# Performance work log

Hardware: AMD Instinct MI355X
Metric: run time of the kernel (lower is better)

## Reference

```python
import jax, jax.numpy as jnp
import numpy as np

# Mamba2 hyperparams (mamba_ssm defaults given __init__ args)
D_MODEL = 512
FF = 2048
D_STATE = 128
D_CONV = 4
EXPAND = 2
D_INNER = EXPAND * D_MODEL          # 1024
HEADDIM = 64
NHEADS = D_INNER // HEADDIM         # 16
NGROUPS = 1
CONV_DIM = D_INNER + 2 * NGROUPS * D_STATE       # 1280
D_IN_PROJ = 2 * D_INNER + 2 * NGROUPS * D_STATE + NHEADS  # 2320
CHUNK = 128
EPS = 1e-5


def setup_inputs() -> dict:
    key = jax.random.key(0)
    ks = jax.random.split(key, 16)
    B, S = 8, 2048
    s = 0.02
    dt_init = jax.random.uniform(ks[4], (NHEADS,), minval=0.001, maxval=0.1)
    return {
        # forward args (dropout treated as eval / identity)
        "tgt": jax.random.normal(ks[0], (B, S, D_MODEL), jnp.float32),
        "memory": jax.random.normal(ks[1], (B, 256, D_MODEL), jnp.float32),
        "spatial_shapes": jnp.array([[16, 16]], jnp.int32),
        "level_start_index": jnp.array([0], jnp.int32),
        "valid_ratios": jnp.ones((B, 1, 2), jnp.float32),
        # Mamba2 params
        "in_proj_w": jax.random.normal(ks[2], (D_IN_PROJ, D_MODEL), jnp.float32) * s,
        "conv_w": jax.random.normal(ks[3], (CONV_DIM, D_CONV), jnp.float32) * s,
        "conv_b": jnp.zeros((CONV_DIM,), jnp.float32),
        "dt_bias": jnp.log(jnp.expm1(dt_init)),  # inverse softplus of dt_init
        "A_log": jnp.log(jax.random.uniform(ks[5], (NHEADS,), minval=1.0, maxval=16.0)),
        "D_head": jnp.ones((NHEADS,), jnp.float32),
        "norm_w": jnp.ones((D_INNER,), jnp.float32),
        "out_proj_w": jax.random.normal(ks[6], (D_MODEL, D_INNER), jnp.float32) * s,
        # LayerNorms + FFN
        "norm1_w": jnp.ones((D_MODEL,)), "norm1_b": jnp.zeros((D_MODEL,)),
        "w1": jax.random.normal(ks[7], (FF, D_MODEL), jnp.float32) * s,
        "b1": jnp.zeros((FF,)),
        "w2": jax.random.normal(ks[8], (D_MODEL, FF), jnp.float32) * s,
        "b2": jnp.zeros((D_MODEL,)),
        "norm3_w": jnp.ones((D_MODEL,)), "norm3_b": jnp.zeros((D_MODEL,)),
    }


def _layer_norm(x, w, b):
    m = jnp.mean(x, -1, keepdims=True)
    v = jnp.mean((x - m) ** 2, -1, keepdims=True)
    return (x - m) * jax.lax.rsqrt(v + EPS) * w + b


def _ssd(x, dt, A, Bm, Cm):
    # chunked selective-scan (SSD). x:(b,s,h,p) dt:(b,s,h) A:(h,) Bm,Cm:(b,s,n)
    b, s, h, p = x.shape
    n = Bm.shape[-1]
    c, l = s // CHUNK, CHUNK
    x = x.reshape(b, c, l, h, p)
    dt = dt.reshape(b, c, l, h)
    Bm = Bm.reshape(b, c, l, n)
    Cm = Cm.reshape(b, c, l, n)
    a_cs = jnp.cumsum(dt * A, axis=2)                 # (b,c,l,h) cumulative log-decay
    ac = a_cs.transpose(0, 1, 3, 2)                   # (b,c,h,l)
    mask = jnp.tril(jnp.ones((l, l), bool))
    Lmat = jnp.exp(jnp.where(mask, ac[..., :, None] - ac[..., None, :], -jnp.inf))
    # intra-chunk (causal) contribution
    Y_diag = jnp.einsum('bcin,bcjn,bchij,bcjh,bcjhp->bcihp', Cm, Bm, Lmat, dt, x)
    # per-chunk final states
    decay_end = jnp.exp(a_cs[:, :, -1:, :] - a_cs)    # (b,c,l,h)
    states = jnp.einsum('bcln,bclh,bclh,bclhp->bchpn', Bm, decay_end, dt, x)
    chunk_decay = jnp.exp(a_cs[:, :, -1, :])          # (b,c,h)
    def step(h0, inp):
        cd, st = inp
        return cd[:, :, None, None] * h0 + st, h0
    h_init = jnp.zeros((b, h, p, n), x.dtype)
    _, prev = jax.lax.scan(step, h_init,
                           (chunk_decay.transpose(1, 0, 2),
                            states.transpose(1, 0, 2, 3, 4)))
    prev = prev.transpose(1, 0, 2, 3, 4)              # (b,c,h,p,n) state at chunk start
    Y_off = jnp.einsum('bcln,bchpn,bclh->bclhp', Cm, prev, jnp.exp(a_cs))
    return (Y_diag + Y_off).reshape(b, s, h, p)


def _mamba2(u, in_proj_w, conv_w, conv_b, dt_bias, A_log, D_head, norm_w, out_proj_w):
    Bb, S, _ = u.shape
    zxbcdt = u @ in_proj_w.T                          # (b,s,2320)
    z, xBC, dt = jnp.split(zxbcdt, [D_INNER, D_INNER + CONV_DIM], axis=-1)
    # causal depthwise conv1d + silu
    xp = jnp.pad(xBC, ((0, 0), (D_CONV - 1, 0), (0, 0)))
    conv = sum(xp[:, k:k + S, :] * conv_w[:, k] for k in range(D_CONV)) + conv_b
    xBC = jax.nn.silu(conv)
    x, Bm, Cm = jnp.split(xBC, [D_INNER, D_INNER + NGROUPS * D_STATE], axis=-1)
    dt = jax.nn.softplus(dt + dt_bias)                # (b,s,h)
    A = -jnp.exp(A_log)                               # (h,)
    x = x.reshape(Bb, S, NHEADS, HEADDIM)
    y = _ssd(x, dt, A, Bm, Cm) + D_head[None, None, :, None] * x
    y = y.reshape(Bb, S, D_INNER)
    # gated RMSNorm: rmsnorm(y * silu(z)) * w
    y = y * jax.nn.silu(z)
    y = y * jax.lax.rsqrt(jnp.mean(y * y, -1, keepdims=True) + EPS) * norm_w
    return y @ out_proj_w.T


def reference(tgt, memory, spatial_shapes, level_start_index, valid_ratios,
              in_proj_w, conv_w, conv_b, dt_bias, A_log, D_head, norm_w, out_proj_w,
              norm1_w, norm1_b, w1, b1, w2, b2, norm3_w, norm3_b):
    t2 = _mamba2(tgt, in_proj_w, conv_w, conv_b, dt_bias, A_log, D_head, norm_w, out_proj_w)
    t = _layer_norm(tgt + t2, norm1_w, norm1_b)
    ff = jax.nn.gelu(t @ w1.T + b1, approximate=False) @ w2.T + b2
    return _layer_norm(t + ff, norm3_w, norm3_b)
```

## Files before the change

### kernel.cpp

```cpp
#include <hip/hip_runtime.h>
#include <hip/hip_bf16.h>
#include <math.h>


namespace {
constexpr int BB = 8;
constexpr int S = 2048;
constexpr int DM = 512;
constexpr int DIP = 2320;
constexpr int DIPP = 2432;
constexpr int DI = 1024;
constexpr int CDIM = 1280;
constexpr int NH = 16;
constexpr int HD = 64;
constexpr int DSTATE = 128;
constexpr int CH = 128;
constexpr int NC = S / CH;
constexpr int FF = 2048;
constexpr float EPS = 1e-5f;
constexpr int LP = 132;
}

using bf16_t = __hip_bfloat16;
typedef __attribute__((ext_vector_type(8))) short short8;
typedef __attribute__((ext_vector_type(4))) float f32x4;

__device__ __forceinline__ float gelu_exact(float x) {
    return 0.5f * x * (1.0f + erff(x * 0.7071067811865476f));
}
__device__ __forceinline__ unsigned short f2bfu(float f) {
    bf16_t b = __float2bfloat16(f);
    return *(unsigned short*)&b;
}
__device__ __forceinline__ float bfu2f(unsigned short u) {
    union { unsigned int i; float f; } v; v.i = (unsigned)u << 16; return v.f;
}

__device__ __forceinline__ void block_sum2(float& a, float& b) {
    #pragma unroll
    for (int o = 32; o > 0; o >>= 1) {
        a += __shfl_down(a, o, 64);
        b += __shfl_down(b, o, 64);
    }
    __shared__ float sa[4], sb[4];
    int w = threadIdx.x >> 6;
    if ((threadIdx.x & 63) == 0) { sa[w] = a; sb[w] = b; }
    __syncthreads();
    a = sa[0] + sa[1] + sa[2] + sa[3];
    b = sb[0] + sb[1] + sb[2] + sb[3];
}

template <int BM, int BK, int ACT, bool HASBIAS, bool OUTBF>
__global__ __launch_bounds__(256)
void mfma_gemm(const bf16_t* __restrict__ A, const bf16_t* __restrict__ W,
               const float* __restrict__ bias, void* __restrict__ Cout,
               int N, int K, int lda, int ldw, int ldc,
               long batchA, long batchW, long batchC)
{
    A += (long)blockIdx.z * batchA;
    W += (long)blockIdx.z * batchW;
    constexpr int NJ = (BM == 128) ? 4 : 2;
    constexpr int KO = BK / 32;
    constexpr int QA = 256 / BM;
    constexpr int TA = (BM * BK) / 2048;
    constexpr int TW = (128 * BK) / 2048;
    __shared__ bf16_t As[2][BM * BK];
    __shared__ bf16_t Ws[2][128 * BK];
    const int tid = threadIdx.x;
    const int lane = tid & 63;
    const int wave = tid >> 6;

    const int nwg = gridDim.x * gridDim.y;
    int wgid = blockIdx.y * gridDim.x + blockIdx.x;
    if ((nwg & 7) == 0) {
        const int q = nwg >> 3;
        wgid = (wgid & 7) * q + (wgid >> 3);
    }
    const int bxi = wgid % gridDim.x;
    const int byi = wgid / gridDim.x;
    const long bm = (long)byi * BM;
    const int bn = bxi * 128;

    const int rA = tid & (BM - 1);
    const int qA = tid / BM;
    const int rW = tid & 127;
    const int qW = tid >> 7;
    const bf16_t* Ag = A + (bm + rA) * (long)lda + qA * 8;
    const bf16_t* Wg = W + ((long)bn + rW) * (long)ldw + qW * 8;
    const int laoff = (qA * BM + rA) * 8;
    const int lwoff = (qW * 128 + rW) * 8;

    const int kq = lane >> 4;
    const int lr = lane & 15;
    const int wm = (BM == 128) ? (wave & 1) * 64 : 0;
    const int wn = (BM == 128) ? (wave >> 1) * 64 : wave * 32;

    f32x4 acc[4][NJ];
    #pragma unroll
    for (int i = 0; i < 4; i++)
        #pragma unroll
        for (int j = 0; j < NJ; j++) acc[i][j] = (f32x4){0.f, 0.f, 0.f, 0.f};

    short8 raA[TA], rwA[TW];
    short8 raB[TA], rwB[TW];
    const int nt = K / BK;

    #pragma unroll
    for (int u = 0; u < TA; u++) raA[u] = *(const short8*)(Ag + u * (QA * 8));
    #pragma unroll
    for (int u = 0; u < TW; u++) rwA[u] = *(const short8*)(Wg + u * 16);
    #pragma unroll
    for (int u = 0; u < TA; u++) *(short8*)&As[0][laoff + u * (QA * BM * 8)] = raA[u];
    #pragma unroll
    for (int u = 0; u < TW; u++) *(short8*)&Ws[0][lwoff + u * 2048] = rwA[u];
    if (nt > 1) {
        #pragma unroll
        for (int u = 0; u < TA; u++) raB[u] = *(const short8*)(Ag + BK + u * (QA * 8));
        #pragma unroll
        for (int u = 0; u < TW; u++) rwB[u] = *(const short8*)(Wg + BK + u * 16);
    }

    for (int t = 0; t < nt; t += 2) {
        if (t + 2 < nt) {
            const long ko = (long)(t + 2) * BK;
            #pragma unroll
            for (int u = 0; u < TA; u++) raA[u] = *(const short8*)(Ag + ko + u * (QA * 8));
            #pragma unroll
            for (int u = 0; u < TW; u++) rwA[u] = *(const short8*)(Wg + ko + u * 16);
        }
        __syncthreads();
        #pragma unroll
        for (int hk = 0; hk < KO; hk++) {
            short8 af[4], bfr[NJ];
            #pragma unroll
            for (int i = 0; i < 4; i++)
                af[i] = *(const short8*)&As[0][((hk * 4 + kq) * BM + wm + i * 16 + lr) * 8];
            #pragma unroll
            for (int j = 0; j < NJ; j++)
                bfr[j] = *(const short8*)&Ws[0][((hk * 4 + kq) * 128 + wn + j * 16 + lr) * 8];
            #pragma unroll
            for (int i = 0; i < 4; i++)
                #pragma unroll
                for (int j = 0; j < NJ; j++)
                    acc[i][j] = __builtin_amdgcn_mfma_f32_16x16x32_bf16(af[i], bfr[j], acc[i][j], 0, 0, 0);
        }
        #pragma unroll
        for (int u = 0; u < TA; u++) *(short8*)&As[1][laoff + u * (QA * BM * 8)] = raB[u];
        #pragma unroll
        for (int u = 0; u < TW; u++) *(short8*)&Ws[1][lwoff + u * 2048] = rwB[u];

        if (t + 3 < nt) {
            const long ko = (long)(t + 3) * BK;
            #pragma unroll
            for (int u = 0; u < TA; u++) raB[u] = *(const short8*)(Ag + ko + u * (QA * 8));
            #pragma unroll
            for (int u = 0; u < TW; u++) rwB[u] = *(const short8*)(Wg + ko + u * 16);
        }
        __syncthreads();
        #pragma unroll
        for (int hk = 0; hk < KO; hk++) {
            short8 af[4], bfr[NJ];
            #pragma unroll
            for (int i = 0; i < 4; i++)
                af[i] = *(const short8*)&As[1][((hk * 4 + kq) * BM + wm + i * 16 + lr) * 8];
            #pragma unroll
            for (int j = 0; j < NJ; j++)
                bfr[j] = *(const short8*)&Ws[1][((hk * 4 + kq) * 128 + wn + j * 16 + lr) * 8];
            #pragma unroll
            for (int i = 0; i < 4; i++)
                #pragma unroll
                for (int j = 0; j < NJ; j++)
                    acc[i][j] = __builtin_amdgcn_mfma_f32_16x16x32_bf16(af[i], bfr[j], acc[i][j], 0, 0, 0);
        }
        if (t + 2 < nt) {
            #pragma unroll
            for (int u = 0; u < TA; u++) *(short8*)&As[0][laoff + u * (QA * BM * 8)] = raA[u];
            #pragma unroll
            for (int u = 0; u < TW; u++) *(short8*)&Ws[0][lwoff + u * 2048] = rwA[u];
        }
    }

    const bool addb = HASBIAS && (blockIdx.z == 0);
    #pragma unroll
    for (int i = 0; i < 4; i++) {
        #pragma unroll
        for (int j = 0; j < NJ; j++) {
            int col = bn + wn + j * 16 + lr;
            if (col < N) {
                float bv = addb ? bias[col] : 0.f;
                #pragma unroll
                for (int r = 0; r < 4; r++) {
                    long row = bm + wm + i * 16 + kq * 4 + r;
                    float v = acc[i][j][r] + bv;
                    if (ACT == 1) v = gelu_exact(v);
                    if (OUTBF) ((bf16_t*)Cout)[row * (long)ldc + col + blockIdx.z * batchC] = __float2bfloat16(v);
                    else       ((float*)Cout)[row * (long)ldc + col + blockIdx.z * batchC] = v;
                }
            }
        }
    }
}

__global__ __launch_bounds__(256)
void dt_cvt(const float* __restrict__ tgt, const float* __restrict__ Wdt,
            const float* __restrict__ dt_bias, bf16_t* __restrict__ tgt_bf,
            float* __restrict__ dts)
{
    const int lane = threadIdx.x & 63;
    const int wave = threadIdx.x >> 6;
    float Wl[16][8];
    #pragma unroll
    for (int h = 0; h < 16; h++) {
        float4 a = *(const float4*)&Wdt[h * 512 + lane * 8];
        float4 b = *(const float4*)&Wdt[h * 512 + lane * 8 + 4];
        Wl[h][0] = a.x; Wl[h][1] = a.y; Wl[h][2] = a.z; Wl[h][3] = a.w;
        Wl[h][4] = b.x; Wl[h][5] = b.y; Wl[h][6] = b.z; Wl[h][7] = b.w;
    }
    float bs[16];
    #pragma unroll
    for (int h = 0; h < 16; h++) bs[h] = dt_bias[h];

    const long row0 = ((long)blockIdx.x * 4 + wave) * 4;
    #pragma unroll
    for (int rr = 0; rr < 4; rr++) {
        const long t = row0 + rr;
        float4 xa = *(const float4*)&tgt[t * 512 + lane * 8];
        float4 xb = *(const float4*)&tgt[t * 512 + lane * 8 + 4];
        float x[8] = {xa.x, xa.y, xa.z, xa.w, xb.x, xb.y, xb.z, xb.w};
        short8 ob;
        #pragma unroll
        for (int q = 0; q < 8; q++) ob[q] = (short)f2bfu(x[q]);
        *(short8*)&tgt_bf[t * 512 + lane * 8] = ob;

        float acc[16];
        #pragma unroll
        for (int h = 0; h < 16; h++) {
            float s = 0.f;
            #pragma unroll
            for (int q = 0; q < 8; q++) s += x[q] * Wl[h][q];
            acc[h] = s;
        }
        #pragma unroll
        for (int off = 32; off > 0; off >>= 1)
            #pragma unroll
            for (int h = 0; h < 16; h++)
                acc[h] += __shfl_xor(acc[h], off, 64);
        if (lane == 0) {
            #pragma unroll
            for (int h = 0; h < 16; h++) {
                float v = acc[h] + bs[h];
                dts[t * NH + h] = (v > 20.f) ? v : log1pf(__expf(v));
            }
        }
    }
}

__global__ __launch_bounds__(256)
void cvt_bf16(const float* __restrict__ s, bf16_t* __restrict__ d, long n)
{
    long i = ((long)blockIdx.x * 256 + threadIdx.x) * 4;
    if (i >= n) return;
    float4 v = *(const float4*)(s + i);
    d[i + 0] = __float2bfloat16(v.x);
    d[i + 1] = __float2bfloat16(v.y);
    d[i + 2] = __float2bfloat16(v.z);
    d[i + 3] = __float2bfloat16(v.w);
}

__global__ __launch_bounds__(256)
void cvt_bf16_pad(const float* __restrict__ s, bf16_t* __restrict__ d,
                  int rows_src, long total, int cols)
{
    long i = (long)blockIdx.x * 256 + threadIdx.x;
    if (i >= total) return;
    long r = i / cols;
    d[i] = __float2bfloat16(r < rows_src ? s[i] : 0.f);
}

__global__ __launch_bounds__(256)
void conv_silu_t16(const bf16_t* __restrict__ zx, const float* __restrict__ cw,
                   const float* __restrict__ cb, bf16_t* __restrict__ xBC)
{
    const int quad = blockIdx.x * 64 + (threadIdx.x & 63);
    const int wv = threadIdx.x >> 6;
    const int c = quad * 4;
    const int s0 = blockIdx.y * 64 + wv * 16;
    const long t0 = (long)blockIdx.z * S + s0;

    float wgt[4][4];
    #pragma unroll
    for (int cc = 0; cc < 4; cc++)
        #pragma unroll
        for (int k = 0; k < 4; k++) wgt[cc][k] = cw[(c + cc) * 4 + k];
    float bias[4];
    #pragma unroll
    for (int cc = 0; cc < 4; cc++) bias[cc] = cb[c + cc];

    unsigned long long rows[19];
    #pragma unroll
    for (int i = 0; i < 19; i++) {
        int s = s0 + i - 3;
        rows[i] = (s >= 0) ? *(const unsigned long long*)&zx[(t0 + i - 3) * DIP + DI + c] : 0ULL;
    }
    #pragma unroll
    for (int i = 0; i < 16; i++) {
        float v[4];
        #pragma unroll
        for (int cc = 0; cc < 4; cc++) v[cc] = bias[cc];
        #pragma unroll
        for (int k = 0; k < 4; k++) {
            unsigned long long u = rows[i + k];
            v[0] += bfu2f((unsigned short)(u      )) * wgt[0][k];
            v[1] += bfu2f((unsigned short)(u >> 16)) * wgt[1][k];
            v[2] += bfu2f((unsigned short)(u >> 32)) * wgt[2][k];
            v[3] += bfu2f((unsigned short)(u >> 48)) * wgt[3][k];
        }
        unsigned long long o = 0;
        #pragma unroll
        for (int cc = 0; cc < 4; cc++) {
            float sv = v[cc] / (1.f + __expf(-v[cc]));
            o |= (unsigned long long)f2bfu(sv) << (16 * cc);
        }
        *(unsigned long long*)&xBC[(t0 + i) * (long)CDIM + c] = o;
    }
}

__global__ __launch_bounds__(256)
void ssd_states(const bf16_t* __restrict__ xBC, const float* __restrict__ dts,
                const float* __restrict__ A_log,
                float* __restrict__ st, float* __restrict__ acs_all,
                float* __restrict__ cdlog)
{
    const int bid = blockIdx.x;
    const int nh = bid & 1;
    const int h = (bid >> 1) & 15;
    const int c = (bid >> 5) & 15;
    const int b = bid >> 9;
    const int sbid = (b * NC + c) * NH + h;
    const int tid = threadIdx.x;
    const int lane = tid & 63;
    const int wave = tid >> 6;
    __shared__ float dtv[128];
    __shared__ float acs[128];
    __shared__ float wj[128];
    __shared__ bf16_t XT[64 * LP];
    __shared__ bf16_t BwT[64 * LP];
    const long t0 = (long)b * S + (long)c * CH;
    const float Ah = -__expf(A_log[h]);

    if (tid < 128) {
        float d = dts[(t0 + tid) * NH + h];
        dtv[tid] = d;
        acs[tid] = d * Ah;
    }
    __syncthreads();
    for (int off = 1; off < 128; off <<= 1) {
        float add = 0.f;
        if (tid < 128 && tid >= off) add = acs[tid - off];
        __syncthreads();
        if (tid < 128 && tid >= off) acs[tid] += add;
        __syncthreads();
    }
    const float el = acs[127];
    if (tid < 128) wj[tid] = __expf(el - acs[tid]) * dtv[tid];
    if (nh == 0) {
        if (tid < 128) acs_all[(long)sbid * 128 + tid] = acs[tid];
        if (tid == 0) cdlog[sbid] = el;
    }
    __syncthreads();

    const int n0b = nh * 64;
    for (int i = tid; i < 4096; i += 256) {
        int p = i & 63, jp = (i >> 6) << 1;
        unsigned short a = *(const unsigned short*)&xBC[(t0 + jp) * CDIM + h * HD + p];
        unsigned short bb = *(const unsigned short*)&xBC[(t0 + jp + 1) * CDIM + h * HD + p];
        *(unsigned int*)&XT[p * LP + jp] = (unsigned)a | ((unsigned)bb << 16);
    }
    for (int i = tid; i < 4096; i += 256) {
        int n = i & 63, jp = (i >> 6) << 1;
        float v0 = __bfloat162float(xBC[(t0 + jp) * CDIM + DI + n0b + n]) * wj[jp];
        float v1 = __bfloat162float(xBC[(t0 + jp + 1) * CDIM + DI + n0b + n]) * wj[jp + 1];
        *(unsigned int*)&BwT[n * LP + jp] = (unsigned)f2bfu(v0) | ((unsigned)f2bfu(v1) << 16);
    }
    __syncthreads();

    const int kq = lane >> 4;
    const int lr = lane & 15;
    const int p0w = (wave & 1) * 32;
    const int n0w = (wave >> 1) * 32;
    f32x4 acc[2][2];
    #pragma unroll
    for (int i = 0; i < 2; i++)
        #pragma unroll
        for (int j = 0; j < 2; j++) acc[i][j] = (f32x4){0.f, 0.f, 0.f, 0.f};
    #pragma unroll
    for (int t = 0; t < 4; t++) {
        short8 af[2], bfr[2];
        #pragma unroll
        for (int i = 0; i < 2; i++)
            af[i] = *(const short8*)&XT[(p0w + i * 16 + lr) * LP + t * 32 + kq * 8];
        #pragma unroll
        for (int j = 0; j < 2; j++)
            bfr[j] = *(const short8*)&BwT[(n0w + j * 16 + lr) * LP + t * 32 + kq * 8];
        #pragma unroll
        for (int i = 0; i < 2; i++)
            #pragma unroll
            for (int j = 0; j < 2; j++)
                acc[i][j] = __builtin_amdgcn_mfma_f32_16x16x32_bf16(af[i], bfr[j], acc[i][j], 0, 0, 0);
    }
    long base = (long)sbid * 8192;
    #pragma unroll
    for (int i = 0; i < 2; i++)
        #pragma unroll
        for (int j = 0; j < 2; j++) {
            int col = n0b + n0w + j * 16 + lr;
            #pragma unroll
            for (int r = 0; r < 4; r++) {
                int p = p0w + i * 16 + kq * 4 + r;
                st[base + p * 128 + col] = acc[i][j][r];
            }
        }
}

__global__ __launch_bounds__(256)
void ssd_scan(const float* __restrict__ st, const float* __restrict__ cdlog,
              bf16_t* __restrict__ prevb)
{
    const int h = blockIdx.x & 15;
    const int b = blockIdx.x >> 4;
    const int q0 = blockIdx.y * 8;
    const int tid = threadIdx.x;
    float prev[8];
    #pragma unroll
    for (int q = 0; q < 8; q++) prev[q] = 0.f;
    for (int c = 0; c < NC; c++) {
        int bc = (b * NC + c) * NH + h;
        float cd = __expf(cdlog[bc]);
        long base = (long)bc * 8192 + (long)q0 * 256;
        #pragma unroll
        for (int q = 0; q < 8; q++) {
            long idx = base + (long)q * 256 + tid;
            float v = st[idx];
            prevb[idx] = __float2bfloat16(prev[q]);
            prev[q] = cd * prev[q] + v;
        }
    }
}

__global__ __launch_bounds__(256)
void ssd_out(const bf16_t* __restrict__ xBC, const float* __restrict__ dts,
             const bf16_t* __restrict__ G, const bf16_t* __restrict__ prevb,
             const float* __restrict__ acs_all, const float* __restrict__ D_head,
             bf16_t* __restrict__ y)
{
    const int bid = blockIdx.x;
    const int ih = bid & 1;
    const int h = (bid >> 1) & 15;
    const int c = (bid >> 5) & 15;
    const int b = bid >> 9;
    const int sbid = (b * NC + c) * NH + h;
    const int tid = threadIdx.x;
    const int lane = tid & 63;
    const int wave = tid >> 6;
    __shared__ float dtv[128];
    __shared__ float acs[128];
    __shared__ float eacs[64];
    __shared__ bf16_t Abuf[64 * LP];
    __shared__ bf16_t Bbuf[64 * LP];
    const long t0 = (long)b * S + (long)c * CH;
    const int m0b = ih * 64;

    if (tid < 128) {
        dtv[tid] = dts[(t0 + tid) * NH + h];
        acs[tid] = acs_all[(long)sbid * 128 + tid];
    }
    __syncthreads();
    if (tid < 64) eacs[tid] = __expf(acs[m0b + tid]);

    const bf16_t* Gb = G + (long)(b * NC + c) * 128 * 128;
    for (int i = tid; i < 4096; i += 256) {
        int rl = i >> 6, kp = (i & 63) << 1;
        int grow = m0b + rl;
        unsigned int g2 = *(const unsigned int*)&Gb[grow * 128 + kp];
        float w0 = (kp     <= grow) ? bfu2f((unsigned short)(g2      )) * __expf(acs[grow] - acs[kp    ]) * dtv[kp    ] : 0.f;
        float w1 = (kp + 1 <= grow) ? bfu2f((unsigned short)(g2 >> 16)) * __expf(acs[grow] - acs[kp + 1]) * dtv[kp + 1] : 0.f;
        *(unsigned int*)&Abuf[rl * LP + kp] = (unsigned)f2bfu(w0) | ((unsigned)f2bfu(w1) << 16);
    }
    for (int i = tid; i < 4096; i += 256) {
        int p = i & 63, jp = (i >> 6) << 1;
        unsigned short a = *(const unsigned short*)&xBC[(t0 + jp) * CDIM + h * HD + p];
        unsigned short bb = *(const unsigned short*)&xBC[(t0 + jp + 1) * CDIM + h * HD + p];
        *(unsigned int*)&Bbuf[p * LP + jp] = (unsigned)a | ((unsigned)bb << 16);
    }
    __syncthreads();

    const int kq = lane >> 4;
    const int lr = lane & 15;
    const int m0w = (wave & 1) * 32;
    const int p0 = (wave >> 1) * 32;
    f32x4 acc[2][2];
    #pragma unroll
    for (int i = 0; i < 2; i++)
        #pragma unroll
        for (int j = 0; j < 2; j++) acc[i][j] = (f32x4){0.f, 0.f, 0.f, 0.f};

    #pragma unroll
    for (int t = 0; t < 4; t++) {
        short8 af[2], bfr[2];
        #pragma unroll
        for (int i = 0; i < 2; i++)
            af[i] = *(const short8*)&Abuf[(m0w + i * 16 + lr) * LP + t * 32 + kq * 8];
        #pragma unroll
        for (int j = 0; j < 2; j++)
            bfr[j] = *(const short8*)&Bbuf[(p0 + j * 16 + lr) * LP + t * 32 + kq * 8];
        #pragma unroll
        for (int i = 0; i < 2; i++)
            #pragma unroll
            for (int j = 0; j < 2; j++)
                acc[i][j] = __builtin_amdgcn_mfma_f32_16x16x32_bf16(af[i], bfr[j], acc[i][j], 0, 0, 0);
    }
    const float Dh = D_head[h];
    float dx[2][2][4];
    #pragma unroll
    for (int i = 0; i < 2; i++)
        #pragma unroll
        for (int j = 0; j < 2; j++) {
            int col = p0 + j * 16 + lr;
            #pragma unroll
            for (int r = 0; r < 4; r++) {
                int rl = m0w + i * 16 + kq * 4 + r;
                dx[i][j][r] = Dh * __bfloat162float(Bbuf[col * LP + m0b + rl]);
            }
        }
    __syncthreads();

    for (int i = tid; i < 4096; i += 256) {
        int rl = i >> 6, np = (i & 63) << 1;
        unsigned int c2 = *(const unsigned int*)&xBC[(t0 + m0b + rl) * CDIM + DI + DSTATE + np];
        float e = eacs[rl];
        float v0 = e * bfu2f((unsigned short)(c2      ));
        float v1 = e * bfu2f((unsigned short)(c2 >> 16));
        *(unsigned int*)&Abuf[rl * LP + np] = (unsigned)f2bfu(v0) | ((unsigned)f2bfu(v1) << 16);
    }
    for (int i = tid; i < 4096; i += 256) {
        int p = i >> 6, np = (i & 63) << 1;
        *(unsigned int*)&Bbuf[p * LP + np] =
            *(const unsigned int*)&prevb[(long)sbid * 8192 + p * 128 + np];
    }
    __syncthreads();

    #pragma unroll
    for (int t = 0; t < 4; t++) {
        short8 af[2], bfr[2];
        #pragma unroll
        for (int i = 0; i < 2; i++)
            af[i] = *(const short8*)&Abuf[(m0w + i * 16 + lr) * LP + t * 32 + kq * 8];
        #pragma unroll
        for (int j = 0; j < 2; j++)
            bfr[j] = *(const short8*)&Bbuf[(p0 + j * 16 + lr) * LP + t * 32 + kq * 8];
        #pragma unroll
        for (int i = 0; i < 2; i++)
            #pragma unroll
            for (int j = 0; j < 2; j++)
                acc[i][j] = __builtin_amdgcn_mfma_f32_16x16x32_bf16(af[i], bfr[j], acc[i][j], 0, 0, 0);
    }

    #pragma unroll
    for (int i = 0; i < 2; i++)
        #pragma unroll
        for (int j = 0; j < 2; j++) {
            int col = p0 + j * 16 + lr;
            #pragma unroll
            for (int r = 0; r < 4; r++) {
                int rl = m0w + i * 16 + kq * 4 + r;
                y[(t0 + m0b + rl) * DI + h * HD + col] = __float2bfloat16(acc[i][j][r] + dx[i][j][r]);
            }
        }
}

__global__ __launch_bounds__(256)
void gated_rms(const bf16_t* __restrict__ y, const bf16_t* __restrict__ zx,
               const float* __restrict__ norm_w, bf16_t* __restrict__ yn)
{
    const long t = blockIdx.x;
    const int d = threadIdx.x * 4;
    unsigned long long zu = *(const unsigned long long*)&zx[t * DIP + d];
    unsigned long long yu = *(const unsigned long long*)&y[t * DI + d];
    float g[4];
    float ss = 0.f, dummy = 0.f;
    #pragma unroll
    for (int q = 0; q < 4; q++) {
        float zv = bfu2f((unsigned short)(zu >> (16 * q)));
        float yv = bfu2f((unsigned short)(yu >> (16 * q)));
        float gv = yv * (zv / (1.f + __expf(-zv)));
        g[q] = gv;
        ss += gv * gv;
    }
    block_sum2(ss, dummy);
    float scale = rsqrtf(ss * (1.f / DI) + EPS);
    unsigned long long o = 0;
    #pragma unroll
    for (int q = 0; q < 4; q++)
        o |= (unsigned long long)f2bfu(g[q] * scale * norm_w[d + q]) << (16 * q);
    *(unsigned long long*)&yn[t * DI + d] = o;
}

template <bool W16>
__global__ __launch_bounds__(256)
void add_ln(const float* __restrict__ x, const float* __restrict__ r,
            const float* __restrict__ w, const float* __restrict__ bpar,
            float* __restrict__ o32, bf16_t* __restrict__ o16)
{
    const int tid = threadIdx.x;
    const long t = blockIdx.x * 2 + (tid >> 7);
    const int i = (tid & 127) * 4;
    float4 xv = *(const float4*)(x + t * DM + i);
    float4 rv = *(const float4*)(r + t * DM + i);
    float v[4] = {xv.x + rv.x, xv.y + rv.y, xv.z + rv.z, xv.w + rv.w};
    float s = v[0] + v[1] + v[2] + v[3];
    float s2 = v[0]*v[0] + v[1]*v[1] + v[2]*v[2] + v[3]*v[3];
    #pragma unroll
    for (int o = 32; o > 0; o >>= 1) {
        s += __shfl_down(s, o, 64);
        s2 += __shfl_down(s2, o, 64);
    }
    __shared__ float sa[4], sb[4];
    int wv = tid >> 6;
    if ((tid & 63) == 0) { sa[wv] = s; sb[wv] = s2; }
    __syncthreads();
    int base = (tid >> 7) * 2;
    s = sa[base] + sa[base + 1];
    s2 = sb[base] + sb[base + 1];
    float mean = s * (1.f / DM);
    float var = s2 * (1.f / DM) - mean * mean;
    float inv = rsqrtf(var + EPS);
    float4 ov;
    float* op = (float*)&ov;
    unsigned long long o16u = 0;
    #pragma unroll
    for (int q = 0; q < 4; q++) {
        float o = (v[q] - mean) * inv * w[i + q] + bpar[i + q];
        op[q] = o;
        if (W16) o16u |= (unsigned long long)f2bfu(o) << (16 * q);
    }
    *(float4*)(o32 + t * DM + i) = ov;
    if (W16) *(unsigned long long*)&o16[t * DM + i] = o16u;
}


extern "C" void kernel_launch(void* const* d_in, const int* in_sizes, int n_in,
                              void* d_out, int out_size, void* d_ws, size_t ws_size,
                              hipStream_t stream)
{
    const float* tgt       = (const float*)d_in[0];
    const float* in_proj_w = (const float*)d_in[5];
    const float* conv_w    = (const float*)d_in[6];
    const float* conv_b    = (const float*)d_in[7];
    const float* dt_bias   = (const float*)d_in[8];
    const float* A_log     = (const float*)d_in[9];
    const float* D_head    = (const float*)d_in[10];
    const float* norm_w    = (const float*)d_in[11];
    const float* out_proj_w= (const float*)d_in[12];
    const float* norm1_w   = (const float*)d_in[13];
    const float* norm1_b   = (const float*)d_in[14];
    const float* w1        = (const float*)d_in[15];
    const float* b1        = (const float*)d_in[16];
    const float* w2        = (const float*)d_in[17];
    const float* b2        = (const float*)d_in[18];
    const float* norm3_w   = (const float*)d_in[19];
    const float* norm3_b   = (const float*)d_in[20];
    float* out = (float*)d_out;

    float* ws = (float*)d_ws;

    const size_t SZ_INW  = (size_t)DIPP * DM / 2;
    const size_t SZ_OUTW = (size_t)DM * DI / 2;
    const size_t SZ_W1   = (size_t)FF * DM / 2;
    const size_t SZ_W2   = (size_t)DM * FF / 2;
    size_t wo = 0;
    bf16_t* inW  = (bf16_t*)(ws + wo); wo += SZ_INW;
    bf16_t* outW = (bf16_t*)(ws + wo); wo += SZ_OUTW;
    bf16_t* w1b  = (bf16_t*)(ws + wo); wo += SZ_W1;
    bf16_t* w2b  = (bf16_t*)(ws + wo); wo += SZ_W2;
    const size_t WB = wo;

    const size_t PB = (size_t)S * DM / 2
                    + (size_t)S * DIP / 2
                    + (size_t)S * NH
                    + (size_t)S * CDIM / 2
                    + (size_t)NC * 128 * 128 / 2
                    + (size_t)NC * NH * 128
                    + (size_t)NC * NH
                    + (size_t)S * DI
                    + (size_t)S * DI;
    int NB = 0;
    for (int nb = 8; nb >= 1; nb >>= 1) {
        if (ws_size >= (WB + (size_t)nb * PB) * sizeof(float)) { NB = nb; break; }
    }
    if (NB == 0) return;

    {
        long n = (long)DIPP * DM;
        cvt_bf16_pad<<<(n + 255) / 256, 256, 0, stream>>>(in_proj_w, inW, DIP, n, DM);
        n = (long)DM * DI;
        cvt_bf16<<<(n / 4 + 255) / 256, 256, 0, stream>>>(out_proj_w, outW, n);
        n = (long)FF * DM;
        cvt_bf16<<<(n / 4 + 255) / 256, 256, 0, stream>>>(w1, w1b, n);
        n = (long)DM * FF;
        cvt_bf16<<<(n / 4 + 255) / 256, 256, 0, stream>>>(w2, w2b, n);
    }

    for (int b0 = 0; b0 < BB; b0 += NB) {
        const long Tg = (long)NB * S;
        size_t o = WB;
        bf16_t* tgt_bf = (bf16_t*)(ws + o); o += (size_t)Tg * DM / 2;
        bf16_t* zx     = (bf16_t*)(ws + o); o += (size_t)Tg * DIP / 2;
        float*  dts    = ws + o;            o += (size_t)Tg * NH;
        bf16_t* xBC    = (bf16_t*)(ws + o); o += (size_t)Tg * CDIM / 2;
        bf16_t* Gbuf   = (bf16_t*)(ws + o); o += (size_t)NB * NC * 128 * 128 / 2;
        float*  acs    = ws + o;            o += (size_t)NB * NC * NH * 128;
        float*  cdl    = ws + o;            o += (size_t)NB * NC * NH;
        float*  ybuf   = ws + o;            o += (size_t)Tg * DI;
        float*  st     = ws + o;            o += (size_t)Tg * DI;

        bf16_t* ybf   = (bf16_t*)ybuf;
        bf16_t* prevb = (bf16_t*)(ybuf + (size_t)Tg * DI / 2);
        bf16_t* yn  = (bf16_t*)st;
        float*  t2  = ybuf;
        float*  tb  = (float*)zx;
        bf16_t* tbb = (bf16_t*)(((float*)zx) + Tg * DM);
        bf16_t* h1  = (bf16_t*)ybuf;
        float*  fb  = (float*)xBC;

        const float* tgt_g = tgt + (long)b0 * S * DM;
        float* out_g = out + (long)b0 * S * DM;

        dt_cvt<<<Tg / 16, 256, 0, stream>>>(
            tgt_g, in_proj_w + (long)(DI + CDIM) * DM, dt_bias, tgt_bf, dts);
        mfma_gemm<128, 32, 0, false, true><<<dim3(DIPP / 128, Tg / 128, 1), 256, 0, stream>>>(
            tgt_bf, inW, nullptr, zx, DIP, DM, DM, DM, DIP, 0, 0, 0);
        conv_silu_t16<<<dim3(CDIM / 256, S / 64, NB), 256, 0, stream>>>(zx, conv_w, conv_b, xBC);
        mfma_gemm<128, 32, 0, false, true><<<dim3(1, 1, NB * NC), 256, 0, stream>>>(
            xBC + DI + DSTATE, xBC + DI, nullptr, Gbuf,
            128, DSTATE, CDIM, CDIM, 128,
            (long)CH * CDIM, (long)CH * CDIM, (long)128 * 128);
        ssd_states<<<NB * NC * NH * 2, 256, 0, stream>>>(xBC, dts, A_log, st, acs, cdl);
        ssd_scan<<<dim3(NB * NH, 4), 256, 0, stream>>>(st, cdl, prevb);
        ssd_out<<<NB * NC * NH * 2, 256, 0, stream>>>(xBC, dts, Gbuf, prevb, acs, D_head, ybf);
        gated_rms<<<Tg, 256, 0, stream>>>(ybf, zx, norm_w, yn);
        mfma_gemm<128, 32, 0, false, false><<<dim3(DM / 128, Tg / 128, 1), 256, 0, stream>>>(
            yn, outW, nullptr, t2, DM, DI, DI, DI, DM, 0, 0, 0);
        add_ln<true><<<Tg / 2, 256, 0, stream>>>(tgt_g, t2, norm1_w, norm1_b, tb, tbb);
        mfma_gemm<128, 32, 1, true, true><<<dim3(FF / 128, Tg / 128, 1), 256, 0, stream>>>(
            tbb, w1b, b1, h1, FF, DM, DM, DM, FF, 0, 0, 0);
        mfma_gemm<128, 32, 0, true, false><<<dim3(DM / 128, Tg / 128, 1), 256, 0, stream>>>(
            h1, w2b, b2, fb, DM, FF, FF, FF, DM, 0, 0, 0);
        add_ln<false><<<Tg / 2, 256, 0, stream>>>(tb, fb, norm3_w, norm3_b, out_g, nullptr);
    }
}
```

Before: 824.4 us.

## Merge SSD state and output half-blocks into one block per chunk-head

The SSD state and output kernels previously split each (batch, chunk, head) across two blocks. Each of those blocks redid the cumsum, the X transpose, and the G-weighting and D-term work for its half. Now a single block covers the whole 128-wide tile, with each wave computing a 2x4 MFMA tile, so the shared loads and exp computations are done once. The cumsum also switches from a shared-memory Hillis-Steele loop with many barriers to wave shuffles plus one cross-wave fixup. In exchange the grid has half as many blocks and each block uses more LDS and registers, which can lower occupancy and latency hiding.

```diff
diff --git a/kernel.cpp b/kernel.cpp
--- a/kernel.cpp
+++ b/kernel.cpp
@@ -326,16 +326,15 @@
 }
 
 __global__ __launch_bounds__(256)
-void ssd_states(const bf16_t* __restrict__ xBC, const float* __restrict__ dts,
-                const float* __restrict__ A_log,
-                float* __restrict__ st, float* __restrict__ acs_all,
-                float* __restrict__ cdlog)
+void ssd_states2(const bf16_t* __restrict__ xBC, const float* __restrict__ dts,
+                 const float* __restrict__ A_log,
+                 float* __restrict__ st, float* __restrict__ acs_all,
+                 float* __restrict__ cdlog)
 {
     const int bid = blockIdx.x;
-    const int nh = bid & 1;
-    const int h = (bid >> 1) & 15;
-    const int c = (bid >> 5) & 15;
-    const int b = bid >> 9;
+    const int h = bid & 15;
+    const int c = (bid >> 4) & 15;
+    const int b = bid >> 8;
     const int sbid = (b * NC + c) * NH + h;
     const int tid = threadIdx.x;
     const int lane = tid & 63;
@@ -343,43 +342,45 @@
     __shared__ float dtv[128];
     __shared__ float acs[128];
     __shared__ float wj[128];
+    __shared__ float wsum[2];
     __shared__ bf16_t XT[64 * LP];
-    __shared__ bf16_t BwT[64 * LP];
+    __shared__ bf16_t BwT[128 * LP];
     const long t0 = (long)b * S + (long)c * CH;
     const float Ah = -__expf(A_log[h]);
 
+    float dv = 0.f, x = 0.f;
     if (tid < 128) {
-        float d = dts[(t0 + tid) * NH + h];
-        dtv[tid] = d;
-        acs[tid] = d * Ah;
-    }
-    __syncthreads();
-    for (int off = 1; off < 128; off <<= 1) {
-        float add = 0.f;
-        if (tid < 128 && tid >= off) add = acs[tid - off];
-        __syncthreads();
-        if (tid < 128 && tid >= off) acs[tid] += add;
-        __syncthreads();
-    }
+        dv = dts[(t0 + tid) * NH + h];
+        x = dv * Ah;
+    }
+    #pragma unroll
+    for (int off = 1; off < 64; off <<= 1) {
+        float n = __shfl_up(x, off, 64);
+        if (lane >= off) x += n;
+    }
+    if (tid < 128 && lane == 63) wsum[tid >> 6] = x;
+    __syncthreads();
+    if (tid >= 64 && tid < 128) x += wsum[0];
+    if (tid < 128) { dtv[tid] = dv; acs[tid] = x; }
+    __syncthreads();
     const float el = acs[127];
-    if (tid < 128) wj[tid] = __expf(el - acs[tid]) * dtv[tid];
-    if (nh == 0) {
-        if (tid < 128) acs_all[(long)sbid * 128 + tid] = acs[tid];
-        if (tid == 0) cdlog[sbid] = el;
-    }
-    __syncthreads();
-
-    const int n0b = nh * 64;
+    if (tid < 128) {
+        wj[tid] = __expf(el - acs[tid]) * dtv[tid];
+        acs_all[(long)sbid * 128 + tid] = acs[tid];
+    }
+    if (tid == 0) cdlog[sbid] = el;
+    __syncthreads();
+
     for (int i = tid; i < 4096; i += 256) {
         int p = i & 63, jp = (i >> 6) << 1;
         unsigned short a = *(const unsigned short*)&xBC[(t0 + jp) * CDIM + h * HD + p];
         unsigned short bb = *(const unsigned short*)&xBC[(t0 + jp + 1) * CDIM + h * HD + p];
         *(unsigned int*)&XT[p * LP + jp] = (unsigned)a | ((unsigned)bb << 16);
     }
-    for (int i = tid; i < 4096; i += 256) {
-        int n = i & 63, jp = (i >> 6) << 1;
-        float v0 = __bfloat162float(xBC[(t0 + jp) * CDIM + DI + n0b + n]) * wj[jp];
-        float v1 = __bfloat162float(xBC[(t0 + jp + 1) * CDIM + DI + n0b + n]) * wj[jp + 1];
+    for (int i = tid; i < 8192; i += 256) {
+        int n = i & 127, jp = (i >> 7) << 1;
+        float v0 = __bfloat162float(xBC[(t0 + jp) * CDIM + DI + n]) * wj[jp];
+        float v1 = __bfloat162float(xBC[(t0 + jp + 1) * CDIM + DI + n]) * wj[jp + 1];
         *(unsigned int*)&BwT[n * LP + jp] = (unsigned)f2bfu(v0) | ((unsigned)f2bfu(v1) << 16);
     }
     __syncthreads();
@@ -387,33 +388,33 @@
     const int kq = lane >> 4;
     const int lr = lane & 15;
     const int p0w = (wave & 1) * 32;
-    const int n0w = (wave >> 1) * 32;
-    f32x4 acc[2][2];
+    const int n0w = (wave >> 1) * 64;
+    f32x4 acc[2][4];
     #pragma unroll
     for (int i = 0; i < 2; i++)
         #pragma unroll
-        for (int j = 0; j < 2; j++) acc[i][j] = (f32x4){0.f, 0.f, 0.f, 0.f};
+        for (int j = 0; j < 4; j++) acc[i][j] = (f32x4){0.f, 0.f, 0.f, 0.f};
     #pragma unroll
     for (int t = 0; t < 4; t++) {
-        short8 af[2], bfr[2];
+        short8 af[2], bfr[4];
         #pragma unroll
         for (int i = 0; i < 2; i++)
             af[i] = *(const short8*)&XT[(p0w + i * 16 + lr) * LP + t * 32 + kq * 8];
         #pragma unroll
-        for (int j = 0; j < 2; j++)
+        for (int j = 0; j < 4; j++)
             bfr[j] = *(const short8*)&BwT[(n0w + j * 16 + lr) * LP + t * 32 + kq * 8];
         #pragma unroll
         for (int i = 0; i < 2; i++)
             #pragma unroll
-            for (int j = 0; j < 2; j++)
+            for (int j = 0; j < 4; j++)
                 acc[i][j] = __builtin_amdgcn_mfma_f32_16x16x32_bf16(af[i], bfr[j], acc[i][j], 0, 0, 0);
     }
     long base = (long)sbid * 8192;
     #pragma unroll
     for (int i = 0; i < 2; i++)
         #pragma unroll
-        for (int j = 0; j < 2; j++) {
-            int col = n0b + n0w + j * 16 + lr;
+        for (int j = 0; j < 4; j++) {
+            int col = n0w + j * 16 + lr;
             #pragma unroll
             for (int r = 0; r < 4; r++) {
                 int p = p0w + i * 16 + kq * 4 + r;
@@ -448,42 +449,39 @@
 }
 
 __global__ __launch_bounds__(256)
-void ssd_out(const bf16_t* __restrict__ xBC, const float* __restrict__ dts,
-             const bf16_t* __restrict__ G, const bf16_t* __restrict__ prevb,
-             const float* __restrict__ acs_all, const float* __restrict__ D_head,
-             bf16_t* __restrict__ y)
+void ssd_out2(const bf16_t* __restrict__ xBC, const float* __restrict__ dts,
+              const bf16_t* __restrict__ G, const bf16_t* __restrict__ prevb,
+              const float* __restrict__ acs_all, const float* __restrict__ D_head,
+              bf16_t* __restrict__ y)
 {
     const int bid = blockIdx.x;
-    const int ih = bid & 1;
-    const int h = (bid >> 1) & 15;
-    const int c = (bid >> 5) & 15;
-    const int b = bid >> 9;
+    const int h = bid & 15;
+    const int c = (bid >> 4) & 15;
+    const int b = bid >> 8;
     const int sbid = (b * NC + c) * NH + h;
     const int tid = threadIdx.x;
     const int lane = tid & 63;
     const int wave = tid >> 6;
     __shared__ float dtv[128];
     __shared__ float acs[128];
-    __shared__ float eacs[64];
-    __shared__ bf16_t Abuf[64 * LP];
+    __shared__ float eacs[128];
+    __shared__ bf16_t Abuf[128 * LP];
     __shared__ bf16_t Bbuf[64 * LP];
     const long t0 = (long)b * S + (long)c * CH;
-    const int m0b = ih * 64;
 
     if (tid < 128) {
         dtv[tid] = dts[(t0 + tid) * NH + h];
         acs[tid] = acs_all[(long)sbid * 128 + tid];
     }
     __syncthreads();
-    if (tid < 64) eacs[tid] = __expf(acs[m0b + tid]);
+    if (tid < 128) eacs[tid] = __expf(acs[tid]);
 
     const bf16_t* Gb = G + (long)(b * NC + c) * 128 * 128;
-    for (int i = tid; i < 4096; i += 256) {
+    for (int i = tid; i < 8192; i += 256) {
         int rl = i >> 6, kp = (i & 63) << 1;
-        int grow = m0b + rl;
-        unsigned int g2 = *(const unsigned int*)&Gb[grow * 128 + kp];
-        float w0 = (kp     <= grow) ? bfu2f((unsigned short)(g2      )) * __expf(acs[grow] - acs[kp    ]) * dtv[kp    ] : 0.f;
-        float w1 = (kp + 1 <= grow) ? bfu2f((unsigned short)(g2 >> 16)) * __expf(acs[grow] - acs[kp + 1]) * dtv[kp + 1] : 0.f;
+        unsigned int g2 = *(const unsigned int*)&Gb[rl * 128 + kp];
+        float w0 = (kp     <= rl) ? bfu2f((unsigned short)(g2      )) * __expf(acs[rl] - acs[kp    ]) * dtv[kp    ] : 0.f;
+        float w1 = (kp + 1 <= rl) ? bfu2f((unsigned short)(g2 >> 16)) * __expf(acs[rl] - acs[kp + 1]) * dtv[kp + 1] : 0.f;
         *(unsigned int*)&Abuf[rl * LP + kp] = (unsigned)f2bfu(w0) | ((unsigned)f2bfu(w1) << 16);
     }
     for (int i = tid; i < 4096; i += 256) {
@@ -496,47 +494,46 @@
 
     const int kq = lane >> 4;
     const int lr = lane & 15;
-    const int m0w = (wave & 1) * 32;
-    const int p0 = (wave >> 1) * 32;
-    f32x4 acc[2][2];
+    const int m0w = wave * 32;
+    f32x4 acc[2][4];
     #pragma unroll
     for (int i = 0; i < 2; i++)
         #pragma unroll
-        for (int j = 0; j < 2; j++) acc[i][j] = (f32x4){0.f, 0.f, 0.f, 0.f};
+        for (int j = 0; j < 4; j++) acc[i][j] = (f32x4){0.f, 0.f, 0.f, 0.f};
 
     #pragma unroll
     for (int t = 0; t < 4; t++) {
-        short8 af[2], bfr[2];
+        short8 af[2], bfr[4];
         #pragma unroll
         for (int i = 0; i < 2; i++)
             af[i] = *(const short8*)&Abuf[(m0w + i * 16 + lr) * LP + t * 32 + kq * 8];
         #pragma unroll
-        for (int j = 0; j < 2; j++)
-            bfr[j] = *(const short8*)&Bbuf[(p0 + j * 16 + lr) * LP + t * 32 + kq * 8];
+        for (int j = 0; j < 4; j++)
+            bfr[j] = *(const short8*)&Bbuf[(j * 16 + lr) * LP + t * 32 + kq * 8];
         #pragma unroll
         for (int i = 0; i < 2; i++)
             #pragma unroll
-            for (int j = 0; j < 2; j++)
+            for (int j = 0; j < 4; j++)
                 acc[i][j] = __builtin_amdgcn_mfma_f32_16x16x32_bf16(af[i], bfr[j], acc[i][j], 0, 0, 0);
     }
     const float Dh = D_head[h];
-    float dx[2][2][4];
+    float dx[2][4][4];
     #pragma unroll
     for (int i = 0; i < 2; i++)
         #pragma unroll
-        for (int j = 0; j < 2; j++) {
-            int col = p0 + j * 16 + lr;
+        for (int j = 0; j < 4; j++) {
+            int col = j * 16 + lr;
             #pragma unroll
             for (int r = 0; r < 4; r++) {
                 int rl = m0w + i * 16 + kq * 4 + r;
-                dx[i][j][r] = Dh * __bfloat162float(Bbuf[col * LP + m0b + rl]);
+                dx[i][j][r] = Dh * __bfloat162float(Bbuf[col * LP + rl]);
             }
         }
     __syncthreads();
 
-    for (int i = tid; i < 4096; i += 256) {
+    for (int i = tid; i < 8192; i += 256) {
         int rl = i >> 6, np = (i & 63) << 1;
-        unsigned int c2 = *(const unsigned int*)&xBC[(t0 + m0b + rl) * CDIM + DI + DSTATE + np];
+        unsigned int c2 = *(const unsigned int*)&xBC[(t0 + rl) * CDIM + DI + DSTATE + np];
         float e = eacs[rl];
         float v0 = e * bfu2f((unsigned short)(c2      ));
         float v1 = e * bfu2f((unsigned short)(c2 >> 16));
@@ -551,29 +548,29 @@
 
     #pragma unroll
     for (int t = 0; t < 4; t++) {
-        short8 af[2], bfr[2];
+        short8 af[2], bfr[4];
         #pragma unroll
         for (int i = 0; i < 2; i++)
             af[i] = *(const short8*)&Abuf[(m0w + i * 16 + lr) * LP + t * 32 + kq * 8];
         #pragma unroll
-        for (int j = 0; j < 2; j++)
-            bfr[j] = *(const short8*)&Bbuf[(p0 + j * 16 + lr) * LP + t * 32 + kq * 8];
+        for (int j = 0; j < 4; j++)
+            bfr[j] = *(const short8*)&Bbuf[(j * 16 + lr) * LP + t * 32 + kq * 8];
         #pragma unroll
         for (int i = 0; i < 2; i++)
             #pragma unroll
-            for (int j = 0; j < 2; j++)
+            for (int j = 0; j < 4; j++)
                 acc[i][j] = __builtin_amdgcn_mfma_f32_16x16x32_bf16(af[i], bfr[j], acc[i][j], 0, 0, 0);
     }
 
     #pragma unroll
     for (int i = 0; i < 2; i++)
         #pragma unroll
-        for (int j = 0; j < 2; j++) {
-            int col = p0 + j * 16 + lr;
+        for (int j = 0; j < 4; j++) {
+            int col = j * 16 + lr;
             #pragma unroll
             for (int r = 0; r < 4; r++) {
                 int rl = m0w + i * 16 + kq * 4 + r;
-                y[(t0 + m0b + rl) * DI + h * HD + col] = __float2bfloat16(acc[i][j][r] + dx[i][j][r]);
+                y[(t0 + rl) * DI + h * HD + col] = __float2bfloat16(acc[i][j][r] + dx[i][j][r]);
             }
         }
 }
@@ -744,9 +741,9 @@
             xBC + DI + DSTATE, xBC + DI, nullptr, Gbuf,
             128, DSTATE, CDIM, CDIM, 128,
             (long)CH * CDIM, (long)CH * CDIM, (long)128 * 128);
-        ssd_states<<<NB * NC * NH * 2, 256, 0, stream>>>(xBC, dts, A_log, st, acs, cdl);
+        ssd_states2<<<NB * NC * NH, 256, 0, stream>>>(xBC, dts, A_log, st, acs, cdl);
         ssd_scan<<<dim3(NB * NH, 4), 256, 0, stream>>>(st, cdl, prevb);
-        ssd_out<<<NB * NC * NH * 2, 256, 0, stream>>>(xBC, dts, Gbuf, prevb, acs, D_head, ybf);
+        ssd_out2<<<NB * NC * NH, 256, 0, stream>>>(xBC, dts, Gbuf, prevb, acs, D_head, ybf);
         gated_rms<<<Tg, 256, 0, stream>>>(ybf, zx, norm_w, yn);
         mfma_gemm<128, 32, 0, false, false><<<dim3(DM / 128, Tg / 128, 1), 256, 0, stream>>>(
             yn, outW, nullptr, t2, DM, DI, DI, DI, DM, 0, 0, 0);
```

New measurement: 851.2 us. +3.3%, slower.
